# Kernel tuning notes

Hardware: AMD Instinct MI355X
Metric: run time of the kernel (lower is better)

## Reference

```python
import math
import jax, jax.numpy as jnp
import numpy as np

B, T, C = 8, 1024, 768
H = 12
D = C // H  # 64


def setup_inputs() -> dict:
    key = jax.random.key(0)
    k1, k2, k3, k4, k5 = jax.random.split(key, 5)
    s = 0.02
    return {
        "x": jax.random.normal(k1, (B, T, C), dtype=jnp.float32),
        "w_qkv": jax.random.normal(k2, (C, 3 * C), dtype=jnp.float32) * s,
        "b_qkv": jax.random.normal(k3, (3 * C,), dtype=jnp.float32) * s,
        "w_proj": jax.random.normal(k4, (C, C), dtype=jnp.float32) * s,
        "b_proj": jax.random.normal(k5, (C,), dtype=jnp.float32) * s,
    }


def reference(x, w_qkv, b_qkv, w_proj, b_proj):
    b, t, c = x.shape
    qkv = x @ w_qkv + b_qkv                      # [B,T,3C]
    q, k, v = jnp.split(qkv, 3, axis=-1)
    # [B,T,C] -> [B,H,T,D]
    q = q.reshape(b, t, H, D).transpose(0, 2, 1, 3)
    k = k.reshape(b, t, H, D).transpose(0, 2, 1, 3)
    v = v.reshape(b, t, H, D).transpose(0, 2, 1, 3)
    scale = 1.0 / math.sqrt(D)
    att = jnp.einsum("bhqd,bhkd->bhqk", q, k) * scale   # [B,H,T,T]
    causal = jnp.tril(jnp.ones((t, t), dtype=bool))
    att = jnp.where(causal, att, -jnp.inf)
    att = jax.nn.softmax(att, axis=-1)
    y = jnp.einsum("bhqk,bhkd->bhqd", att, v)            # [B,H,T,D]
    y = y.transpose(0, 2, 1, 3).reshape(b, t, c)
    return y @ w_proj + b_proj
```

## Files before the change

### kernel.cpp

```cpp
#include <hip/hip_runtime.h>
#include <math.h>

#define B_ 8
#define T_ 1024
#define C_ 768
#define H_ 12
#define D_ 64

typedef __bf16 bf16x8 __attribute__((ext_vector_type(8)));
typedef float  f32x4  __attribute__((ext_vector_type(4)));
typedef unsigned short us8 __attribute__((ext_vector_type(8)));
typedef unsigned int   u32x4v __attribute__((ext_vector_type(4)));

typedef __attribute__((address_space(3))) void lds_void;
typedef __attribute__((address_space(1))) const void glb_void;

#define KSC 0.18033688011112043f

__device__ __forceinline__ unsigned short f2bf(float f) {
    unsigned int u = __float_as_uint(f);
    u += 0x7fffu + ((u >> 16) & 1u);
    return (unsigned short)(u >> 16);
}

__global__ __launch_bounds__(256)
void prep_w(const float* __restrict__ x,
            const float* __restrict__ w_qkv, const float* __restrict__ b_qkv,
            const float* __restrict__ w_proj,
            unsigned short* __restrict__ wqT, unsigned short* __restrict__ wpT,
            float* __restrict__ bqs, unsigned short* __restrict__ xb) {
    __shared__ unsigned short Ts[64][65];
    const int id  = blockIdx.x;
    const int tid = threadIdx.x;
    if (id >= 577) {
        const int xid = id - 577;
        const float4* xi = (const float4*)x;
        ushort4* xo = (ushort4*)xb;
#pragma unroll
        for (int it = 0; it < 6; it++) {
            const int idx = (xid * 6 + it) * 256 + tid;
            float4 v = xi[idx];
            ushort4 o;
            o.x = f2bf(v.x); o.y = f2bf(v.y); o.z = f2bf(v.z); o.w = f2bf(v.w);
            xo[idx] = o;
        }
        return;
    }
    if (id == 576) {
        for (int i = tid; i < 3 * C_; i += 256)
            bqs[i] = b_qkv[i] * (i < C_ ? KSC : 1.f);
        return;
    }
    const float* W; unsigned short* Wt; int N, nlim, t2;
    if (id < 432) { t2 = id;       W = w_qkv;  Wt = wqT; N = 3 * C_; nlim = C_; }
    else          { t2 = id - 432; W = w_proj; Wt = wpT; N = C_;     nlim = 0;  }
    const int ntiles = N / 64;
    const int n0 = (t2 % ntiles) * 64, k0 = (t2 / ntiles) * 64;
    for (int i = tid; i < 4096; i += 256) {
        int n = i & 63, k = i >> 6;
        float sc = (n0 + n < nlim) ? KSC : 1.f;
        Ts[n][k] = f2bf(W[(size_t)(k0 + k) * N + n0 + n] * sc);
    }
    __syncthreads();
    for (int i = tid; i < 4096; i += 256) {
        int k = i & 63, n = i >> 6;
        Wt[(size_t)(n0 + n) * 768 + k0 + k] = Ts[n][k];
    }
}

template<int OUT_BF16>
__global__ __launch_bounds__(256, 2)
void gemm_pipe(const unsigned short* __restrict__ A16,
               const unsigned short* __restrict__ Bt, const float* __restrict__ bias,
               void* __restrict__ Cout, int M, int N, int K) {
    __shared__ __align__(16) unsigned short As[8192];
    __shared__ __align__(16) unsigned short Bs[6144];

    const int tid  = threadIdx.x;
    const int lane = tid & 63;
    const int c    = lane & 15;
    const int quad = lane >> 4;
    const int wave = tid >> 6;
    const int wm   = (wave >> 1) * 64;
    const int wn   = (wave & 1) * 48;
    const int bm   = blockIdx.x * 128;
    const int bn   = blockIdx.y * 96;

    const unsigned short* aS[4];
    const unsigned short* bS[3];
#pragma unroll
    for (int p = 0; p < 4; p++) {
        const int Lp = p * 256 + tid;
        const int L  = Lp ^ ((Lp >> 3) & 7);
        aS[p] = A16 + (size_t)(bm + (L >> 3)) * K + (L & 7) * 8;
    }
#pragma unroll
    for (int p = 0; p < 3; p++) {
        const int Lp = p * 256 + tid;
        const int L  = Lp ^ ((Lp >> 3) & 7);
        bS[p] = Bt + (size_t)(bn + (L >> 3)) * K + (L & 7) * 8;
    }
    const int wb = (tid & 0xC0) * 8;

    int aoff[4][2], boff[3][2];
#pragma unroll
    for (int ks = 0; ks < 2; ks++) {
        const int kcA = (ks * 4 + quad) ^ (c & 7);
#pragma unroll
        for (int i = 0; i < 4; i++)
            aoff[i][ks] = ((wm + i * 16 + c) * 8 + kcA) * 8;
#pragma unroll
        for (int j = 0; j < 3; j++)
            boff[j][ks] = ((wn + j * 16 + c) * 8 + kcA) * 8;
    }

    f32x4 acc[4][3];
#pragma unroll
    for (int i = 0; i < 4; i++)
#pragma unroll
        for (int j = 0; j < 3; j++) acc[i][j] = (f32x4){0.f, 0.f, 0.f, 0.f};

#pragma unroll
    for (int p = 0; p < 4; p++) {
        __builtin_amdgcn_global_load_lds((glb_void*)aS[p],
            (lds_void*)(&As[0] + p * 2048 + wb), 16, 0, 0);
        aS[p] += 64;
    }
#pragma unroll
    for (int p = 0; p < 3; p++) {
        __builtin_amdgcn_global_load_lds((glb_void*)bS[p],
            (lds_void*)(&Bs[0] + p * 2048 + wb), 16, 0, 0);
        bS[p] += 64;
    }

    const int R = K >> 6;
    for (int r = 0; r < R; r++) {
        __syncthreads();

#pragma unroll
        for (int ks = 0; ks < 2; ks++) {
            bf16x8 af[4], bfr[3];
#pragma unroll
            for (int i = 0; i < 4; i++)
                af[i] = __builtin_bit_cast(bf16x8, *(const us8*)&As[aoff[i][ks]]);
#pragma unroll
            for (int j = 0; j < 3; j++)
                bfr[j] = __builtin_bit_cast(bf16x8, *(const us8*)&Bs[boff[j][ks]]);
#pragma unroll
            for (int i = 0; i < 4; i++)
#pragma unroll
                for (int j = 0; j < 3; j++)
                    acc[i][j] = __builtin_amdgcn_mfma_f32_16x16x32_bf16(af[i], bfr[j], acc[i][j], 0, 0, 0);
        }

        __syncthreads();

        if (r + 1 < R) {
#pragma unroll
            for (int p = 0; p < 4; p++) {
                __builtin_amdgcn_global_load_lds((glb_void*)aS[p],
                    (lds_void*)(&As[0] + p * 2048 + wb), 16, 0, 0);
                aS[p] += 64;
            }
#pragma unroll
            for (int p = 0; p < 3; p++) {
                __builtin_amdgcn_global_load_lds((glb_void*)bS[p],
                    (lds_void*)(&Bs[0] + p * 2048 + wb), 16, 0, 0);
                bS[p] += 64;
            }
        }
    }

    float bs[3];
#pragma unroll
    for (int j = 0; j < 3; j++) bs[j] = bias[bn + wn + j * 16 + c];
#pragma unroll
    for (int i = 0; i < 4; i++) {
        const int gm = bm + wm + i * 16 + quad * 4;
#pragma unroll
        for (int r = 0; r < 4; r++) {
            const size_t ro = (size_t)(gm + r) * N;
#pragma unroll
            for (int j = 0; j < 3; j++) {
                const float v = acc[i][j][r] + bs[j];
                const int gn = bn + wn + j * 16 + c;
                if (OUT_BF16) ((unsigned short*)Cout)[ro + gn] = f2bf(v);
                else          ((float*)Cout)[ro + gn] = v;
            }
        }
    }
}

__device__ __forceinline__ int sigmaK(int k) {
    return 16 * (2 * (k >> 5) + ((k >> 2) & 1)) + 4 * ((k >> 3) & 3) + (k & 3);
}

__global__ __launch_bounds__(256, 3)
void attn_mfma(const unsigned short* __restrict__ qkv, unsigned short* __restrict__ y) {
    __shared__ __align__(16) unsigned short Ks[64 * 72];
    __shared__ __align__(16) unsigned int   Vt[64 * 36];

    const int tid  = threadIdx.x;
    const int wave = tid >> 6;
    const int lane = tid & 63;
    const int c    = lane & 15;
    const int quad = lane >> 4;

    const int id = blockIdx.x;
    const int p  = (id >> 3) & 7;
    const int bh = (id >> 6) * 8 + (id & 7);
    const int b  = bh / H_;
    const int h  = bh - b * H_;

    const int qts[2] = {p, 15 - p};
    const int q0s[2] = {p * 64, (15 - p) * 64};

    const int RS = 3 * C_;
    const unsigned short* kbase = qkv + (size_t)b * T_ * RS + C_ + h * D_;
    const unsigned short* vbase = qkv + (size_t)b * T_ * RS + 2 * C_ + h * D_;

    const u32x4v onesu = {0x3F803F80u, 0x3F803F80u, 0x3F803F80u, 0x3F803F80u};
    const bf16x8 onesf = __builtin_bit_cast(bf16x8, onesu);

    bf16x8 qf[2][2];
#pragma unroll
    for (int t = 0; t < 2; t++) {
        const unsigned short* qrow =
            qkv + ((size_t)(b * T_ + q0s[t] + wave * 16 + c)) * RS + h * D_ + quad * 8;
        qf[t][0] = __builtin_bit_cast(bf16x8, *(const us8*)qrow);
        qf[t][1] = __builtin_bit_cast(bf16x8, *(const us8*)(qrow + 32));
    }

    const int kr0 = tid >> 3, kc0 = tid & 7;
    const int sK0 = sigmaK(kr0) * 72 + kc0 * 8;
    const int sK1 = sigmaK(kr0 + 32) * 72 + kc0 * 8;
    const int dg  = tid >> 4, kp0 = tid & 15;

    us8 kA, kB;
    ushort4 vA0, vB0, vA1, vB1;
    {
        kA = *(const us8*)(kbase + (size_t)kr0 * RS + kc0 * 8);
        kB = *(const us8*)(kbase + (size_t)(kr0 + 32) * RS + kc0 * 8);
        const unsigned short* p0 = vbase + (size_t)(2 * kp0) * RS + dg * 4;
        vA0 = *(const ushort4*)p0;  vB0 = *(const ushort4*)(p0 + RS);
        const unsigned short* p1 = vbase + (size_t)(2 * (kp0 + 16)) * RS + dg * 4;
        vA1 = *(const ushort4*)p1;  vB1 = *(const ushort4*)(p1 + RS);
    }

    f32x4 Oa[2][4];
    f32x4 Ol[2];
#pragma unroll
    for (int t = 0; t < 2; t++) {
        Ol[t] = (f32x4){0.f, 0.f, 0.f, 0.f};
#pragma unroll
        for (int d = 0; d < 4; d++) Oa[t][d] = (f32x4){0.f, 0.f, 0.f, 0.f};
    }

    const int ktEnd = qts[1];
    for (int kt = 0; kt <= ktEnd; kt++) {
        __syncthreads();
        *(us8*)&Ks[sK0] = kA;
        *(us8*)&Ks[sK1] = kB;
        {
            unsigned int* v0 = &Vt[(dg * 4) * 36 + kp0];
            v0[0]   = vA0.x | ((unsigned)vB0.x << 16);
            v0[36]  = vA0.y | ((unsigned)vB0.y << 16);
            v0[72]  = vA0.z | ((unsigned)vB0.z << 16);
            v0[108] = vA0.w | ((unsigned)vB0.w << 16);
            unsigned int* v1 = v0 + 16;
            v1[0]   = vA1.x | ((unsigned)vB1.x << 16);
            v1[36]  = vA1.y | ((unsigned)vB1.y << 16);
            v1[72]  = vA1.z | ((unsigned)vB1.z << 16);
            v1[108] = vA1.w | ((unsigned)vB1.w << 16);
        }
        __syncthreads();

        if (kt < ktEnd) {
            const unsigned short* kp = kbase + (size_t)((kt + 1) * 64) * RS;
            kA = *(const us8*)(kp + (size_t)kr0 * RS + kc0 * 8);
            kB = *(const us8*)(kp + (size_t)(kr0 + 32) * RS + kc0 * 8);
            const unsigned short* vp = vbase + (size_t)((kt + 1) * 64) * RS;
            const unsigned short* p0 = vp + (size_t)(2 * kp0) * RS + dg * 4;
            vA0 = *(const ushort4*)p0;  vB0 = *(const ushort4*)(p0 + RS);
            const unsigned short* p1 = vp + (size_t)(2 * (kp0 + 16)) * RS + dg * 4;
            vA1 = *(const ushort4*)p1;  vB1 = *(const ushort4*)(p1 + RS);
        }

        bf16x8 kf[4][2];
#pragma unroll
        for (int nb = 0; nb < 4; nb++) {
#pragma unroll
            for (int ks = 0; ks < 2; ks++)
                kf[nb][ks] = __builtin_bit_cast(bf16x8,
                    *(const us8*)&Ks[(nb * 16 + c) * 72 + quad * 8 + ks * 32]);
        }

#pragma unroll
        for (int t = 0; t < 2; t++) {
            if (kt > qts[t]) continue;
            const bool diag = (kt == qts[t]);
            const bool doHi = !diag || (wave >= 2);
            const int nbmax = diag ? ((wave >= 2) ? 3 : 1) : 3;

            f32x4 sv[4];
            __builtin_amdgcn_s_setprio(1);
#pragma unroll
            for (int nb = 0; nb < 4; nb++) {
                if (nb <= nbmax) {
                    f32x4 z = (f32x4){0.f, 0.f, 0.f, 0.f};
                    z = __builtin_amdgcn_mfma_f32_16x16x32_bf16(kf[nb][0], qf[t][0], z, 0, 0, 0);
                    sv[nb] = __builtin_amdgcn_mfma_f32_16x16x32_bf16(kf[nb][1], qf[t][1], z, 0, 0, 0);
                }
            }
            __builtin_amdgcn_s_setprio(0);
            if (diag) {
                const int qloc = wave * 16 + c;
#pragma unroll
                for (int nb = 0; nb < 4; nb++) {
                    if (nb <= nbmax) {
                        const int kb = 32 * (nb >> 1) + 4 * (nb & 1) + 8 * quad;
#pragma unroll
                        for (int r = 0; r < 4; r++)
                            if (kb + r > qloc) sv[nb][r] = -INFINITY;
                    }
                }
            }

            unsigned int pd[4][2];
#pragma unroll
            for (int nb = 0; nb < 4; nb++) {
                if (nb <= nbmax) {
                    float p0 = __builtin_amdgcn_exp2f(sv[nb][0]);
                    float p1 = __builtin_amdgcn_exp2f(sv[nb][1]);
                    float p2 = __builtin_amdgcn_exp2f(sv[nb][2]);
                    float p3 = __builtin_amdgcn_exp2f(sv[nb][3]);
                    unsigned u0 = __float_as_uint(p0) + 0x8000u;
                    unsigned u1 = __float_as_uint(p1) + 0x8000u;
                    unsigned u2 = __float_as_uint(p2) + 0x8000u;
                    unsigned u3 = __float_as_uint(p3) + 0x8000u;
                    pd[nb][0] = (u0 >> 16) | (u1 & 0xffff0000u);
                    pd[nb][1] = (u2 >> 16) | (u3 & 0xffff0000u);
                } else {
                    pd[nb][0] = 0u; pd[nb][1] = 0u;
                }
            }

            bf16x8 ap0 = __builtin_bit_cast(bf16x8,
                (u32x4v){pd[0][0], pd[0][1], pd[1][0], pd[1][1]});
            bf16x8 ap1 = __builtin_bit_cast(bf16x8,
                (u32x4v){pd[2][0], pd[2][1], pd[3][0], pd[3][1]});

            __builtin_amdgcn_s_setprio(1);
            Ol[t] = __builtin_amdgcn_mfma_f32_16x16x32_bf16(ap0, onesf, Ol[t], 0, 0, 0);
            if (doHi)
                Ol[t] = __builtin_amdgcn_mfma_f32_16x16x32_bf16(ap1, onesf, Ol[t], 0, 0, 0);

#pragma unroll
            for (int dd = 0; dd < 4; dd++) {
                const unsigned int* vrow = &Vt[(dd * 16 + c) * 36 + quad * 4];
                bf16x8 vb0 = __builtin_bit_cast(bf16x8, *(const u32x4v*)vrow);
                Oa[t][dd] = __builtin_amdgcn_mfma_f32_16x16x32_bf16(ap0, vb0, Oa[t][dd], 0, 0, 0);
                if (doHi) {
                    bf16x8 vb1 = __builtin_bit_cast(bf16x8, *(const u32x4v*)(vrow + 16));
                    Oa[t][dd] = __builtin_amdgcn_mfma_f32_16x16x32_bf16(ap1, vb1, Oa[t][dd], 0, 0, 0);
                }
            }
            __builtin_amdgcn_s_setprio(0);
        }
    }

#pragma unroll
    for (int t = 0; t < 2; t++) {
        unsigned short* yrow =
            y + ((size_t)(b * T_ + q0s[t] + wave * 16)) * C_ + h * D_;
#pragma unroll
        for (int r = 0; r < 4; r++) {
            float inv = 1.f / Ol[t][r];
#pragma unroll
            for (int dd = 0; dd < 4; dd++)
                yrow[(size_t)(quad * 4 + r) * C_ + dd * 16 + c] = f2bf(Oa[t][dd][r] * inv);
        }
    }
}

extern "C" void kernel_launch(void* const* d_in, const int* in_sizes, int n_in,
                              void* d_out, int out_size, void* d_ws, size_t ws_size,
                              hipStream_t stream) {
    const float* x      = (const float*)d_in[0];
    const float* w_qkv  = (const float*)d_in[1];
    const float* b_qkv  = (const float*)d_in[2];
    const float* w_proj = (const float*)d_in[3];
    const float* b_proj = (const float*)d_in[4];
    float* out = (float*)d_out;

    unsigned short* wqT  = (unsigned short*)d_ws;
    unsigned short* wpT  = wqT  + (size_t)3 * C_ * C_;
    unsigned short* qkvb = wpT  + (size_t)C_ * C_;
    unsigned short* yb   = qkvb + (size_t)B_ * T_ * 3 * C_;
    float*          bqs  = (float*)(yb + (size_t)B_ * T_ * C_);

    unsigned short* xb = yb;

    prep_w<<<1601, 256, 0, stream>>>(x, w_qkv, b_qkv, w_proj, wqT, wpT, bqs, xb);

    gemm_pipe<1><<<dim3(B_ * T_ / 128, 3 * C_ / 96), 256, 0, stream>>>(
        xb, wqT, bqs, qkvb, B_ * T_, 3 * C_, C_);

    attn_mfma<<<8 * B_ * H_, 256, 0, stream>>>(qkvb, yb);

    gemm_pipe<0><<<dim3(B_ * T_ / 128, C_ / 96), 256, 0, stream>>>(
        yb, wpT, b_proj, out, B_ * T_, C_, C_);
}
```

Before: 170.4 us.

## Use 256x96 tile GEMM kernel for the QKV projection

Adds a new GEMM kernel with a 256-row M tile, where each wave computes 128x48 and holds an 8x3 accumulator array, and uses it for the QKV projection. The larger tile is meant to increase reuse of B fragments and halve the number of B tile loads per output. It is single-buffered with two barriers per K step and larger LDS use, so it gives up the overlap of the previous pipelined kernel. The grid drops to 768 blocks, which risks lower occupancy and latency hiding.

```diff
diff --git a/kernel.cpp b/kernel.cpp
--- a/kernel.cpp
+++ b/kernel.cpp
@@ -65,6 +65,120 @@
     for (int i = tid; i < 4096; i += 256) {
         int k = i & 63, n = i >> 6;
         Wt[(size_t)(n0 + n) * 768 + k0 + k] = Ts[n][k];
+    }
+}
+
+template<int OUT_BF16>
+__global__ __launch_bounds__(256, 3)
+void gemm_big(const unsigned short* __restrict__ A16,
+              const unsigned short* __restrict__ Bt, const float* __restrict__ bias,
+              void* __restrict__ Cout, int M, int N, int K) {
+    __shared__ __align__(16) unsigned short As[16384];
+    __shared__ __align__(16) unsigned short Bs[6144];
+
+    const int tid  = threadIdx.x;
+    const int lane = tid & 63;
+    const int c    = lane & 15;
+    const int quad = lane >> 4;
+    const int wave = tid >> 6;
+    const int wm   = (wave >> 1) * 128;
+    const int wn   = (wave & 1) * 48;
+    const int bm   = blockIdx.x * 256;
+    const int bn   = blockIdx.y * 96;
+
+    const unsigned short* aS0;
+    const unsigned short* bS0;
+    {
+        const int Lp = tid;
+        const int L  = Lp ^ ((Lp >> 3) & 7);
+        aS0 = A16 + (size_t)(bm + (L >> 3)) * K + (L & 7) * 8;
+        bS0 = Bt  + (size_t)(bn + (L >> 3)) * K + (L & 7) * 8;
+    }
+    const int wb = (tid & 0xC0) * 8;
+
+    int aoff[8][2], boff[3][2];
+#pragma unroll
+    for (int ks = 0; ks < 2; ks++) {
+        const int kcA = (ks * 4 + quad) ^ (c & 7);
+#pragma unroll
+        for (int i = 0; i < 8; i++)
+            aoff[i][ks] = ((wm + i * 16 + c) * 8 + kcA) * 8;
+#pragma unroll
+        for (int j = 0; j < 3; j++)
+            boff[j][ks] = ((wn + j * 16 + c) * 8 + kcA) * 8;
+    }
+
+    f32x4 acc[8][3];
+#pragma unroll
+    for (int i = 0; i < 8; i++)
+#pragma unroll
+        for (int j = 0; j < 3; j++) acc[i][j] = (f32x4){0.f, 0.f, 0.f, 0.f};
+
+#define STAGE_BIG()                                                            \
+    {                                                                          \
+        _Pragma("unroll")                                                      \
+        for (int p = 0; p < 8; p++)                                            \
+            __builtin_amdgcn_global_load_lds((glb_void*)(aS0 + (size_t)p * 32 * K), \
+                (lds_void*)(&As[0] + p * 2048 + wb), 16, 0, 0);                \
+        aS0 += 64;                                                             \
+        _Pragma("unroll")                                                      \
+        for (int p = 0; p < 3; p++)                                            \
+            __builtin_amdgcn_global_load_lds((glb_void*)(bS0 + (size_t)p * 32 * K), \
+                (lds_void*)(&Bs[0] + p * 2048 + wb), 16, 0, 0);                \
+        bS0 += 64;                                                             \
+    }
+
+    STAGE_BIG()
+
+    const int R = K >> 6;
+    for (int r = 0; r < R; r++) {
+        __syncthreads();
+
+#pragma unroll
+        for (int ks = 0; ks < 2; ks++) {
+            bf16x8 bfr[3];
+#pragma unroll
+            for (int j = 0; j < 3; j++)
+                bfr[j] = __builtin_bit_cast(bf16x8, *(const us8*)&Bs[boff[j][ks]]);
+#pragma unroll
+            for (int half = 0; half < 2; half++) {
+                bf16x8 af[4];
+#pragma unroll
+                for (int i = 0; i < 4; i++)
+                    af[i] = __builtin_bit_cast(bf16x8,
+                        *(const us8*)&As[aoff[half * 4 + i][ks]]);
+#pragma unroll
+                for (int i = 0; i < 4; i++)
+#pragma unroll
+                    for (int j = 0; j < 3; j++)
+                        acc[half * 4 + i][j] = __builtin_amdgcn_mfma_f32_16x16x32_bf16(
+                            af[i], bfr[j], acc[half * 4 + i][j], 0, 0, 0);
+            }
+        }
+
+        __syncthreads();
+
+        if (r + 1 < R) STAGE_BIG()
+    }
+#undef STAGE_BIG
+
+    float bs[3];
+#pragma unroll
+    for (int j = 0; j < 3; j++) bs[j] = bias[bn + wn + j * 16 + c];
+#pragma unroll
+    for (int i = 0; i < 8; i++) {
+        const int gm = bm + wm + i * 16 + quad * 4;
+#pragma unroll
+        for (int r = 0; r < 4; r++) {
+            const size_t ro = (size_t)(gm + r) * N;
+#pragma unroll
+            for (int j = 0; j < 3; j++) {
+                const float v = acc[i][j][r] + bs[j];
+                const int gn = bn + wn + j * 16 + c;
+                if (OUT_BF16) ((unsigned short*)Cout)[ro + gn] = f2bf(v);
+                else          ((float*)Cout)[ro + gn] = v;
+            }
+        }
     }
 }
 
@@ -403,7 +517,7 @@
 
     prep_w<<<1601, 256, 0, stream>>>(x, w_qkv, b_qkv, w_proj, wqT, wpT, bqs, xb);
 
-    gemm_pipe<1><<<dim3(B_ * T_ / 128, 3 * C_ / 96), 256, 0, stream>>>(
+    gemm_big<1><<<dim3(B_ * T_ / 256, 3 * C_ / 96), 256, 0, stream>>>(
         xb, wqT, bqs, qkvb, B_ * T_, 3 * C_, C_);
 
     attn_mfma<<<8 * B_ * H_, 256, 0, stream>>>(qkvb, yb);
```

Result: no change. 168.5 us (median of 2 runs) (-1.1%).
